# Performance work log

Hardware: AMD Instinct MI355X
Metric: run time of the kernel (lower is better)

The kernel has to match this reference:

```python
import jax, jax.numpy as jnp
import numpy as np

N, D, OUT = 8192, 512, 1

def setup_inputs() -> dict:
    key = jax.random.key(0)
    ks = jax.random.split(key, 7)
    s2 = (2.0 / (D + OUT)) ** 0.5  # GlorotNormal-ish scale
    return {
        "x": jax.random.normal(ks[0], (N, D), jnp.float32),
        "mu_kernel": jax.random.normal(ks[1], (D, OUT), jnp.float32) * s2,
        "rho_kernel": jax.random.normal(ks[2], (D,), jnp.float32) * (2.0 / (D + 1)) ** 0.5,
        "var_kernel": jax.random.normal(ks[3], (D, OUT), jnp.float32) * s2,
        "mu_bias": jax.random.normal(ks[4], (OUT,), jnp.float32) * 0.1,
        "var_bias": jax.random.normal(ks[5], (OUT,), jnp.float32) * 0.1,
        "cov_bias": jax.random.normal(ks[6], (OUT,), jnp.float32) * 0.1,
    }

def reference(x, mu_kernel, rho_kernel, var_kernel, mu_bias, var_bias, cov_bias):
    # mean head: (n, out)
    mu = x @ mu_kernel + mu_bias
    # diagonal variances: softplus(x @ W_v + b_v) + eps, squeezed to (n,)
    d = jax.nn.softplus(x @ var_kernel + var_bias) + 1e-8
    d = jnp.squeeze(d, axis=-1)
    # off-diagonal covariances: sum_k x_i[k]*x_j[k]*rho[k] + cov_bias
    # == (x * rho_kernel) @ x.T  (fused GEMM; avoids the (n,n,d) tile)
    rho = (x * rho_kernel) @ x.T + cov_bias  # (n, n), cov_bias broadcasts (out=1)
    idx = jnp.arange(x.shape[0])
    cov = rho.at[idx, idx].set(d)  # tf.linalg.set_diag
    return (mu, cov)
```

## Files before the change

### kernel.cpp

```cpp
#include <hip/hip_runtime.h>
#include <math.h>

#define AS1 __attribute__((address_space(1)))
#define AS3 __attribute__((address_space(3)))

typedef _Float16 f16x8 __attribute__((ext_vector_type(8)));
typedef float f32x4 __attribute__((ext_vector_type(4)));

#define NROWS 8192
#define DDIM  512

__global__ __launch_bounds__(256) void prep_kernel(
    const float* __restrict__ x,
    const float* __restrict__ muk,
    const float* __restrict__ rho,
    const float* __restrict__ vark,
    const float* __restrict__ mu_bias,
    const float* __restrict__ var_bias,
    float* __restrict__ mu_out,
    _Float16* __restrict__ xh,
    _Float16* __restrict__ ah,
    float* __restrict__ dvec)
{
    const int wave = threadIdx.x >> 6;
    const int lane = threadIdx.x & 63;
    const int row  = blockIdx.x * 4 + wave;
    const int k    = lane * 8;

    const float4 x0 = *(const float4*)(x + (size_t)row * DDIM + k);
    const float4 x1 = *(const float4*)(x + (size_t)row * DDIM + k + 4);
    const float4 m0 = *(const float4*)(muk + k);
    const float4 m1 = *(const float4*)(muk + k + 4);
    const float4 r0 = *(const float4*)(rho + k);
    const float4 r1 = *(const float4*)(rho + k + 4);
    const float4 v0 = *(const float4*)(vark + k);
    const float4 v1 = *(const float4*)(vark + k + 4);

    float xv[8] = {x0.x, x0.y, x0.z, x0.w, x1.x, x1.y, x1.z, x1.w};
    float rv[8] = {r0.x, r0.y, r0.z, r0.w, r1.x, r1.y, r1.z, r1.w};
    float mv[8] = {m0.x, m0.y, m0.z, m0.w, m1.x, m1.y, m1.z, m1.w};
    float vv[8] = {v0.x, v0.y, v0.z, v0.w, v1.x, v1.y, v1.z, v1.w};

    f16x8 hx, ha;
    float dm = 0.f, dv = 0.f;
#pragma unroll
    for (int j = 0; j < 8; ++j) {
        hx[j] = (_Float16)xv[j];
        ha[j] = (_Float16)(xv[j] * rv[j]);
        dm += xv[j] * mv[j];
        dv += xv[j] * vv[j];
    }
    *(f16x8*)(xh + (size_t)row * DDIM + k) = hx;
    *(f16x8*)(ah + (size_t)row * DDIM + k) = ha;

#pragma unroll
    for (int off = 32; off > 0; off >>= 1) {
        dm += __shfl_down(dm, off, 64);
        dv += __shfl_down(dv, off, 64);
    }
    if (lane == 0) {
        mu_out[row] = dm + mu_bias[0];
        float z  = dv + var_bias[0];
        float sp = fmaxf(z, 0.f) + log1pf(expf(-fabsf(z)));
        dvec[row] = sp + 1e-8f;
    }
}

__device__ __forceinline__ void gload_lds16(const void* g, void* l)
{
    __builtin_amdgcn_global_load_lds((AS1 void*)g, (AS3 void*)l, 16, 0, 0);
}

__global__ __launch_bounds__(256) void cov_kernel(
    const _Float16* __restrict__ A,
    const _Float16* __restrict__ B,
    const float* __restrict__ dvec,
    const float* __restrict__ cov_bias,
    float* __restrict__ C)
{
    __shared__ _Float16 As[3][128 * 32];
    __shared__ _Float16 Bs[3][128 * 32];

    const int t    = threadIdx.x;
    const int lane = t & 63;
    const int wave = t >> 6;
    const int wr   = wave >> 1;
    const int wc   = wave & 1;
    const int quad = lane >> 4;
    const int l16  = lane & 15;
    const int xc   = quad ^ ((l16 >> 1) & 3);

    const int bid = blockIdx.x;
    const int tt  = (bid & 7) * (2080 / 8) + (bid >> 3);

    int bi = (int)((sqrtf(8.f * (float)tt + 1.f) - 1.f) * 0.5f);
    while ((bi + 1) * (bi + 2) / 2 <= tt) ++bi;
    while (bi * (bi + 1) / 2 > tt) --bi;
    const int bj = tt - bi * (bi + 1) / 2;

    const int rowBase = bi * 128;
    const int colBase = bj * 128;
    const float cb = cov_bias[0];

    f32x4 acc[4][4] = {};

    const int sr = t >> 2;
    const int sg = (t & 3) ^ ((sr >> 1) & 3);
    const _Float16* ga = A + ((size_t)(rowBase + sr)) * DDIM + sg * 8;
    const _Float16* gb = B + ((size_t)(colBase + sr)) * DDIM + sg * 8;

#define STAGE(kt, s) do {                                            \
        const int _k0 = (kt) * 32;                                   \
        gload_lds16(ga + _k0,             As[s] + t * 8);            \
        gload_lds16(ga + 64 * DDIM + _k0, As[s] + 2048 + t * 8);     \
        gload_lds16(gb + _k0,             Bs[s] + t * 8);            \
        gload_lds16(gb + 64 * DDIM + _k0, Bs[s] + 2048 + t * 8);     \
    } while (0)

    f16x8 af[4], bf[4];

#define DSREAD(s) do {                                                          \
        _Pragma("unroll")                                                       \
        for (int _i = 0; _i < 4; ++_i)                                          \
            af[_i] = *(const f16x8*)(As[s] + (wr * 64 + _i * 16 + l16) * 32 + xc * 8); \
        _Pragma("unroll")                                                       \
        for (int _j = 0; _j < 4; ++_j)                                          \
            bf[_j] = *(const f16x8*)(Bs[s] + (wc * 64 + _j * 16 + l16) * 32 + xc * 8); \
    } while (0)

#define DOMFMA() do {                                                           \
        _Pragma("unroll")                                                       \
        for (int _i = 0; _i < 4; ++_i)                                          \
            _Pragma("unroll")                                                   \
            for (int _j = 0; _j < 4; ++_j)                                      \
                acc[_i][_j] = __builtin_amdgcn_mfma_f32_16x16x32_f16(           \
                    af[_i], bf[_j], acc[_i][_j], 0, 0, 0);                      \
    } while (0)

    STAGE(0, 0);
    STAGE(1, 1);
    STAGE(2, 2);
    asm volatile("s_waitcnt vmcnt(8)" ::: "memory");
    __builtin_amdgcn_s_barrier();

#pragma unroll 1
    for (int kt = 0; kt < 13; ++kt) {
        const int s = kt % 3;
        DSREAD(s);
        asm volatile("s_waitcnt lgkmcnt(0)" ::: "memory");
        __builtin_amdgcn_s_barrier();
        STAGE(kt + 3, s);
        DOMFMA();
        asm volatile("s_waitcnt vmcnt(8)" ::: "memory");
        __builtin_amdgcn_s_barrier();
    }

    DSREAD(1);
    DOMFMA();
    asm volatile("s_waitcnt vmcnt(4)" ::: "memory");
    __builtin_amdgcn_s_barrier();

    DSREAD(2);
    DOMFMA();
    asm volatile("s_waitcnt vmcnt(0)" ::: "memory");
    __builtin_amdgcn_s_barrier();

    DSREAD(0);
    DOMFMA();

#undef STAGE
#undef DSREAD
#undef DOMFMA

    if (bi == bj) {
#pragma unroll
        for (int i = 0; i < 4; ++i) {
            const int grb = rowBase + wr * 64 + i * 16 + quad * 4;
#pragma unroll
            for (int j = 0; j < 4; ++j) {
                const int gc = colBase + wc * 64 + j * 16 + l16;
#pragma unroll
                for (int r = 0; r < 4; ++r) {
                    const int gr = grb + r;
                    float v = acc[i][j][r] + cb;
                    if (gr == gc) v = dvec[gr];
                    C[(size_t)gr * NROWS + gc] = v;
                }
            }
        }
    } else {
#pragma unroll
        for (int i = 0; i < 4; ++i) {
            const int grb = rowBase + wr * 64 + i * 16 + quad * 4;
#pragma unroll
            for (int j = 0; j < 4; ++j) {
                const int gc = colBase + wc * 64 + j * 16 + l16;
#pragma unroll
                for (int r = 0; r < 4; ++r)
                    C[(size_t)(grb + r) * NROWS + gc] = acc[i][j][r] + cb;
            }
        }

#pragma unroll
        for (int j = 0; j < 4; ++j) {
            const int trow = colBase + wc * 64 + j * 16 + l16;
#pragma unroll
            for (int i = 0; i < 4; ++i) {
                const int tcol = rowBase + wr * 64 + i * 16 + quad * 4;
                float4 v;
                v.x = acc[i][j][0] + cb;
                v.y = acc[i][j][1] + cb;
                v.z = acc[i][j][2] + cb;
                v.w = acc[i][j][3] + cb;
                *(float4*)(C + (size_t)trow * NROWS + tcol) = v;
            }
        }
    }
}

extern "C" void kernel_launch(void* const* d_in, const int* in_sizes, int n_in,
                              void* d_out, int out_size, void* d_ws, size_t ws_size,
                              hipStream_t stream)
{
    const float* x     = (const float*)d_in[0];
    const float* muk   = (const float*)d_in[1];
    const float* rho   = (const float*)d_in[2];
    const float* vark  = (const float*)d_in[3];
    const float* mu_b  = (const float*)d_in[4];
    const float* var_b = (const float*)d_in[5];
    const float* cov_b = (const float*)d_in[6];

    float* out = (float*)d_out;

    _Float16* xh = (_Float16*)d_ws;
    _Float16* ah = xh + (size_t)NROWS * DDIM;
    float* dvec  = (float*)(ah + (size_t)NROWS * DDIM);

    prep_kernel<<<NROWS / 4, 256, 0, stream>>>(x, muk, rho, vark, mu_b, var_b,
                                               out, xh, ah, dvec);

    const int nblk = (NROWS / 128) * (NROWS / 128 + 1) / 2;
    cov_kernel<<<nblk, 256, 0, stream>>>(ah, xh, dvec, cov_b, out + NROWS);
}
```

Before: 346.9 us.

## Group triangular tile order into 8x8 super-tiles and use nontemporal output stores

```diff
diff --git a/kernel.cpp b/kernel.cpp
--- a/kernel.cpp
+++ b/kernel.cpp
@@ -91,12 +91,28 @@
     const int xc   = quad ^ ((l16 >> 1) & 3);
 
     const int bid = blockIdx.x;
-    const int tt  = (bid & 7) * (2080 / 8) + (bid >> 3);
-
-    int bi = (int)((sqrtf(8.f * (float)tt + 1.f) - 1.f) * 0.5f);
-    while ((bi + 1) * (bi + 2) / 2 <= tt) ++bi;
-    while (bi * (bi + 1) / 2 > tt) --bi;
-    const int bj = tt - bi * (bi + 1) / 2;
+    const int tt  = (bid & 7) * 260 + (bid >> 3);
+
+    int SI = (int)((sqrtf(1.f + 8.f * (float)tt) - 1.f) * 0.0625f);
+    while (32 * (SI + 1) * (SI + 1) + 4 * (SI + 1) <= tt) ++SI;
+    while (32 * SI * SI + 4 * SI > tt) --SI;
+    const int rem = tt - (32 * SI * SI + 4 * SI);
+    int SJ, ii, jj;
+    if (rem < 64 * SI) {
+        SJ = rem >> 6;
+        const int w = rem & 63;
+        ii = w >> 3;
+        jj = w & 7;
+    } else {
+        const int w = rem - 64 * SI;
+        SJ = SI;
+        ii = (int)((sqrtf(8.f * (float)w + 1.f) - 1.f) * 0.5f);
+        while ((ii + 1) * (ii + 2) / 2 <= w) ++ii;
+        while (ii * (ii + 1) / 2 > w) --ii;
+        jj = w - ii * (ii + 1) / 2;
+    }
+    const int bi = SI * 8 + ii;
+    const int bj = SJ * 8 + jj;
 
     const int rowBase = bi * 128;
     const int colBase = bj * 128;
@@ -184,7 +200,7 @@
                     const int gr = grb + r;
                     float v = acc[i][j][r] + cb;
                     if (gr == gc) v = dvec[gr];
-                    C[(size_t)gr * NROWS + gc] = v;
+                    __builtin_nontemporal_store(v, C + (size_t)gr * NROWS + gc);
                 }
             }
         }
@@ -197,7 +213,8 @@
                 const int gc = colBase + wc * 64 + j * 16 + l16;
 #pragma unroll
                 for (int r = 0; r < 4; ++r)
-                    C[(size_t)(grb + r) * NROWS + gc] = acc[i][j][r] + cb;
+                    __builtin_nontemporal_store(acc[i][j][r] + cb,
+                                                C + (size_t)(grb + r) * NROWS + gc);
             }
         }
 
@@ -207,12 +224,12 @@
 #pragma unroll
             for (int i = 0; i < 4; ++i) {
                 const int tcol = rowBase + wr * 64 + i * 16 + quad * 4;
-                float4 v;
-                v.x = acc[i][j][0] + cb;
-                v.y = acc[i][j][1] + cb;
-                v.z = acc[i][j][2] + cb;
-                v.w = acc[i][j][3] + cb;
-                *(float4*)(C + (size_t)trow * NROWS + tcol) = v;
+                f32x4 v;
+                v[0] = acc[i][j][0] + cb;
+                v[1] = acc[i][j][1] + cb;
+                v[2] = acc[i][j][2] + cb;
+                v[3] = acc[i][j][3] + cb;
+                __builtin_nontemporal_store(v, (f32x4*)(C + (size_t)trow * NROWS + tcol));
             }
         }
     }
```

New measurement: 335.0 us. 1.04x faster.
